# Kernel optimization log

Measured on AMD Instinct MI355X. Metric: run time of the kernel, lower is better.

Reference implementation:

```python
import jax, jax.numpy as jnp
import numpy as np

B = 1024       # batch of triples
E = 50000      # num_entities
R = 500        # num_relations
D = 512        # dimension
P = 16         # parts
C = 8          # num_cores
ALPHA = 2.0    # -> q = alpha/2 = 1.0
Q = ALPHA / 2.0
DP = D // P    # 32


def setup_inputs() -> dict:
    key = jax.random.key(0)
    ks = jax.random.split(key, 10)
    xav_e = (2.0 / (E + D)) ** 0.5
    xav_r = (2.0 / (R + D)) ** 0.5
    return {
        "heads": jax.random.randint(ks[0], (B,), 0, E),
        "relations": jax.random.randint(ks[1], (B,), 0, R),
        "tails": jax.random.randint(ks[2], (B,), 0, E),
        "entity_w": jax.random.normal(ks[3], (E, D), dtype=jnp.float32) * xav_e,
        "relation_w": jax.random.normal(ks[4], (R, D), dtype=jnp.float32) * xav_r,
        "W_cores": jax.random.uniform(ks[5], (C, P, P, P), dtype=jnp.float32,
                                      minval=-0.01, maxval=0.01),
        "attn_w1": jax.random.normal(ks[6], (2 * D, D), dtype=jnp.float32) * (1.0 / (2 * D)) ** 0.5,
        "attn_b1": jnp.zeros((D,), dtype=jnp.float32),
        "attn_w2": jax.random.normal(ks[7], (D, C), dtype=jnp.float32) * (1.0 / D) ** 0.5,
        "attn_b2": jnp.zeros((C,), dtype=jnp.float32),
    }


def _pq_norm(x):
    # ((|x|^p).sum(2) ** q).sum(1), p=2
    return ((x * x).sum(2) ** Q).sum(1)


def _geometric_consistency(W_cores):
    # center of mass of |W| along each axis, per core; vectorized over cores
    coords = jnp.arange(P, dtype=jnp.float32)
    Wa = jnp.abs(W_cores)                      # [C,P,P,P]
    tot = Wa.sum(axis=(1, 2, 3))               # [C]
    cx = (Wa * coords[None, :, None, None]).sum(axis=(1, 2, 3)) / tot
    cy = (Wa * coords[None, None, :, None]).sum(axis=(1, 2, 3)) / tot
    cz = (Wa * coords[None, None, None, :]).sum(axis=(1, 2, 3)) / tot
    centers = jnp.stack([cx, cy, cz], axis=1)  # [C,3]
    d2 = ((centers[:, None, :] - centers[None, :, :]) ** 2).sum(-1)
    dist = jnp.sqrt(d2)
    masked = dist + jnp.eye(C, dtype=dist.dtype) * 1e6
    min_d = masked.min(axis=1)
    return -jnp.mean(jnp.log(min_d + 1e-6))


def reference(heads, relations, tails, entity_w, relation_w, W_cores,
              attn_w1, attn_b1, attn_w2, attn_b2):
    h = entity_w[heads]          # [B,D]
    r = relation_w[relations]    # [B,D]
    t = entity_w[tails]          # [B,D]

    hr = jnp.concatenate([h, r], axis=1)                       # [B,2D]
    hid = jax.nn.relu(hr @ attn_w1 + attn_b1)                  # [B,D]
    attn = jax.nn.softmax(hid @ attn_w2 + attn_b2, axis=1)     # [B,C]

    h3 = h.reshape(-1, DP, P)
    r3 = r.reshape(-1, DP, P)
    t3 = t.reshape(-1, DP, P)

    h_norm = _pq_norm(h3)
    r_norm = _pq_norm(r3)
    t_norm = _pq_norm(t3)

    # attention-weighted effective core per triple (sum over cores is linear,
    # so folding attn into W before the contraction is exactly the same math)
    Weff = jnp.einsum('bc,cpqs->bpqs', attn, W_cores)          # [B,P,P,P]

    # x1[b,i,s] = sum_{p,q} h[b,i,p] r[b,i,q] W[b,p,q,s]
    x1 = jnp.einsum('bip,biq,bpqs->bis', h3, r3, Weff)
    # x2[b,i,p] = sum_{q,s} r[b,i,q] t[b,i,s] W[b,p,q,s]
    x2 = jnp.einsum('biq,bis,bpqs->bip', r3, t3, Weff)
    # x3[b,i,q] = sum_{p,s} h[b,i,p] t[b,i,s] W[b,p,q,s]
    x3 = jnp.einsum('bip,bis,bpqs->biq', h3, t3, Weff)

    whr_norm = _pq_norm(x1)
    wrt_norm = _pq_norm(x2)
    wth_norm = _pq_norm(x3)

    scores = x1.reshape(-1, D) @ entity_w.T                    # [B,E]

    factor1 = jnp.mean(h_norm) + jnp.mean(r_norm) + jnp.mean(t_norm)
    factor2 = jnp.mean(whr_norm) + jnp.mean(wrt_norm) + jnp.mean(wth_norm)
    factor3 = _geometric_consistency(W_cores)
    return (scores, factor1, factor2, factor3, attn)
```

## Files before the change

kernel.cpp:

```cpp
#include <hip/hip_runtime.h>
#include <cstdint>
#include <cstddef>

#define NB 1024
#define NE 50000
#define NE_PAD 50048
#define DCOL 512
#define ATTN_C 8

static const size_t SCORES_OFF = (size_t)NB * NE;
static const size_t F1_OFF = SCORES_OFF + 0;
static const size_t F2_OFF = SCORES_OFF + 1;
static const size_t F3_OFF = SCORES_OFF + 2;
static const size_t ATTN_OFF = SCORES_OFF + 3;

typedef float f32x4 __attribute__((ext_vector_type(4)));
typedef short s16x8 __attribute__((ext_vector_type(8)));

__device__ __forceinline__ unsigned short f2bf(float f) {
  union { float f; uint32_t u; } x; x.f = f;
  uint32_t u = x.u;
  uint32_t r = (u + 0x7fffu + ((u >> 16) & 1u)) >> 16;
  return (unsigned short)r;
}

__device__ __forceinline__ void gload16(const void* g, void* l) {
  __builtin_amdgcn_global_load_lds(
      (const __attribute__((address_space(1))) uint32_t*)g,
      (__attribute__((address_space(3))) uint32_t*)l, 16, 0, 0);
}

template <int N>
__device__ __forceinline__ void waitcnt_vm() {
  static_assert(N == 0 || N == 4 || N == 8, "literal dispatch");
  if constexpr (N == 0) asm volatile("s_waitcnt vmcnt(0)" ::: "memory");
  else if constexpr (N == 4) asm volatile("s_waitcnt vmcnt(4)" ::: "memory");
  else if constexpr (N == 8) asm volatile("s_waitcnt vmcnt(8)" ::: "memory");
}

__global__ __launch_bounds__(256)
void prep(const int* __restrict__ heads, const int* __restrict__ rels,
          const int* __restrict__ tails, const float* __restrict__ ew,
          const float* __restrict__ rw, const float* __restrict__ w1,
          unsigned short* __restrict__ hrb, unsigned short* __restrict__ w1t,
          unsigned short* __restrict__ ewb, float* __restrict__ n1) {
  int tid = threadIdx.x;
  if (blockIdx.x < NB) {
    int b = blockIdx.x;
    const float* h = ew + (size_t)heads[b] * DCOL;
    const float* r = rw + (size_t)rels[b] * DCOL;
    const float* t = ew + (size_t)tails[b] * DCOL;
    float acc = 0.f;
    #pragma unroll
    for (int it = 0; it < 2; ++it) {
      int d = it * 256 + tid;
      float hv = h[d], rv = r[d], tv = t[d];
      hrb[(size_t)b * 1024 + d] = f2bf(hv);
      hrb[(size_t)b * 1024 + DCOL + d] = f2bf(rv);
      acc += hv * hv + rv * rv + tv * tv;
    }
    __shared__ float red[256];
    red[tid] = acc; __syncthreads();
    for (int s = 128; s > 0; s >>= 1) {
      if (tid < s) red[tid] += red[tid + s];
      __syncthreads();
    }
    if (tid == 0) n1[b] = red[0];
  } else if (blockIdx.x < NB + 512) {
    int tb = blockIdx.x - NB;
    int nb = (tb & 15) * 32, kb = (tb >> 4) * 32;
    __shared__ float tile[32][33];
    int tx = tid & 31, ty = tid >> 5;
    #pragma unroll
    for (int rr = 0; rr < 32; rr += 8)
      tile[ty + rr][tx] = w1[(size_t)(kb + ty + rr) * 512 + nb + tx];
    __syncthreads();
    #pragma unroll
    for (int rr = 0; rr < 32; rr += 8)
      w1t[(size_t)(nb + ty + rr) * 1024 + kb + tx] = f2bf(tile[tx][ty + rr]);
  } else {
    const int n4valid = NE * DCOL / 4;
    const int n4tot = NE_PAD * DCOL / 4;
    int i = (blockIdx.x - NB - 512) * 256 + tid;
    const int stride = 2048 * 256;
    for (; i < n4tot; i += stride) {
      float x = 0.f, y = 0.f, z = 0.f, w = 0.f;
      if (i < n4valid) {
        float4 v = ((const float4*)ew)[i];
        x = v.x; y = v.y; z = v.z; w = v.w;
      }
      union { unsigned short u[4]; uint2 v2; } o;
      o.u[0] = f2bf(x); o.u[1] = f2bf(y); o.u[2] = f2bf(z); o.u[3] = f2bf(w);
      ((uint2*)ewb)[i] = o.v2;
    }
  }
}

template <int EPI, int WM, int WN, int FRm, int FRn, int SWZ, int MT>
__global__ __launch_bounds__(WM * WN * 64, WM * WN == 8 ? 4 : 2)
void gemm_nt(const unsigned short* __restrict__ A,
             const unsigned short* __restrict__ B,
             float* __restrict__ C, const float* __restrict__ bias,
             int K, int Nc, int NT) {
  constexpr int NW = WM * WN;
  constexpr int BM = WM * 16 * FRm;
  constexpr int BN = WN * 16 * FRn;
  constexpr int TILE_A = BM * 128;
  constexpr int TILE_B = BN * 128;
  constexpr int BUFSZ = TILE_A + TILE_B;
  constexpr int CPW_A = (BM / 8) / NW;
  constexpr int CPW_B = (BN / 8) / NW;
  constexpr int SOPS = CPW_A + CPW_B;
  static_assert((BM / 8) % NW == 0 && (BN / 8) % NW == 0, "chunk split");
  __shared__ __align__(16) uint8_t smem[2 * BUFSZ];
  const int tid = threadIdx.x;
  const int lane = tid & 63;
  const int wv = tid >> 6;
  const int wm = wv / WN, wn = wv % WN;

  int m_t, n_t;
  if (SWZ) {
    int xcd = blockIdx.x & 7;
    int l = blockIdx.x >> 3;
    int w = xcd * ((MT * NT) >> 3) + l;
    n_t = w / MT; m_t = w % MT;
  } else {
    m_t = blockIdx.x % MT; n_t = blockIdx.x / MT;
  }
  const int m0 = m_t * BM;
  const int n0 = n_t * BN;
  const int rbytes = K * 2;

  f32x4 acc[FRm][FRn];
  #pragma unroll
  for (int i = 0; i < FRm; ++i)
    #pragma unroll
    for (int j = 0; j < FRn; ++j) acc[i][j] = (f32x4){0.f, 0.f, 0.f, 0.f};

  const int srow = lane >> 3;
  const int scol = lane & 7;
  const int nkt = K >> 6;

  auto stage = [&](int kt, int buf) {
    #pragma unroll
    for (int j = 0; j < CPW_A; ++j) {
      const int chunk = wv * CPW_A + j;
      const int r = chunk * 8 + srow;
      const int c = scol ^ (r & 7);
      gload16((const uint8_t*)A + (size_t)(m0 + r) * rbytes + kt * 128 + c * 16,
              &smem[buf * BUFSZ + chunk * 1024]);
    }
    #pragma unroll
    for (int j = 0; j < CPW_B; ++j) {
      const int chunk = wv * CPW_B + j;
      const int r = chunk * 8 + srow;
      const int c = scol ^ (r & 7);
      gload16((const uint8_t*)B + (size_t)(n0 + r) * rbytes + kt * 128 + c * 16,
              &smem[buf * BUFSZ + TILE_A + chunk * 1024]);
    }
  };
  auto compute = [&](int buf) {
    const uint8_t* sa = &smem[buf * BUFSZ];
    const uint8_t* sb = sa + TILE_A;
    #pragma unroll
    for (int kk = 0; kk < 2; ++kk) {
      s16x8 af[FRm], bfv[FRn];
      #pragma unroll
      for (int f = 0; f < FRm; ++f) {
        const int ra = (wm * FRm + f) * 16 + (lane & 15);
        const int ca = (kk * 4 + (lane >> 4)) ^ (ra & 7);
        af[f] = *(const s16x8*)&sa[ra * 128 + ca * 16];
      }
      #pragma unroll
      for (int f = 0; f < FRn; ++f) {
        const int rb = (wn * FRn + f) * 16 + (lane & 15);
        const int cb = (kk * 4 + (lane >> 4)) ^ (rb & 7);
        bfv[f] = *(const s16x8*)&sb[rb * 128 + cb * 16];
      }
      #pragma unroll
      for (int fm = 0; fm < FRm; ++fm)
        #pragma unroll
        for (int fn = 0; fn < FRn; ++fn)
          acc[fm][fn] = __builtin_amdgcn_mfma_f32_16x16x32_bf16(
              af[fm], bfv[fn], acc[fm][fn], 0, 0, 0);
    }
  };

  stage(0, 0);
  stage(1, 1);
  for (int kt = 0; kt < nkt - 1; ++kt) {
    const int cur = kt & 1;
    waitcnt_vm<SOPS>();
    __builtin_amdgcn_sched_barrier(0);
    __builtin_amdgcn_s_barrier();
    __builtin_amdgcn_sched_barrier(0);
    compute(cur);
    __builtin_amdgcn_sched_barrier(0);
    __builtin_amdgcn_s_barrier();
    __builtin_amdgcn_sched_barrier(0);
    if (kt + 2 < nkt) stage(kt + 2, cur);
  }
  waitcnt_vm<0>();
  __builtin_amdgcn_sched_barrier(0);
  __builtin_amdgcn_s_barrier();
  __builtin_amdgcn_sched_barrier(0);
  compute((nkt - 1) & 1);

  const int rl = lane >> 4, cl = lane & 15;
  #pragma unroll
  for (int fm = 0; fm < FRm; ++fm)
    #pragma unroll
    for (int fn = 0; fn < FRn; ++fn)
      #pragma unroll
      for (int j = 0; j < 4; ++j) {
        int gm = m0 + (wm * FRm + fm) * 16 + rl * 4 + j;
        int gn = n0 + (wn * FRn + fn) * 16 + cl;
        if (gn < Nc) {
          float v = acc[fm][fn][j];
          if (EPI) v = fmaxf(v + bias[gn], 0.f);
          C[(size_t)gm * Nc + gn] = v;
        }
      }
}

__global__ __launch_bounds__(256, 2)
void triple_core(const int* __restrict__ heads, const int* __restrict__ rels,
                 const int* __restrict__ tails, const float* __restrict__ ew,
                 const float* __restrict__ rw, const float* __restrict__ wc,
                 const float* __restrict__ hid, const float* __restrict__ w2,
                 const float* __restrict__ b2, float* __restrict__ attn_out,
                 unsigned short* __restrict__ x1b, float* __restrict__ n2) {
  __shared__ float hs[512], rs[512], ts[512];
  __shared__ __align__(16) float W123[4096][4];
  __shared__ float att[8];
  __shared__ float wred[4][8];
  __shared__ float red[256];
  int b = blockIdx.x, tid = threadIdx.x;
  int lane = tid & 63, wid = tid >> 6;
  const float* hp_ = ew + (size_t)heads[b] * DCOL;
  const float* rp_ = rw + (size_t)rels[b] * DCOL;
  const float* tp_ = ew + (size_t)tails[b] * DCOL;
  float la[8] = {0, 0, 0, 0, 0, 0, 0, 0};
  #pragma unroll
  for (int it = 0; it < 2; ++it) {
    int d = it * 256 + tid;
    hs[d] = hp_[d]; rs[d] = rp_[d]; ts[d] = tp_[d];
    float hv = hid[(size_t)b * DCOL + d];
    #pragma unroll
    for (int c = 0; c < 8; ++c) la[c] = fmaf(hv, w2[d * 8 + c], la[c]);
  }
  #pragma unroll
  for (int off = 32; off > 0; off >>= 1)
    #pragma unroll
    for (int c = 0; c < 8; ++c) la[c] += __shfl_down(la[c], off);
  if (lane == 0)
    #pragma unroll
    for (int c = 0; c < 8; ++c) wred[wid][c] = la[c];
  __syncthreads();
  if (tid == 0) {
    float lg[8];
    #pragma unroll
    for (int c = 0; c < 8; ++c)
      lg[c] = wred[0][c] + wred[1][c] + wred[2][c] + wred[3][c] + b2[c];
    float mx = lg[0];
    #pragma unroll
    for (int c = 1; c < 8; ++c) mx = fmaxf(mx, lg[c]);
    float e[8], s = 0.f;
    #pragma unroll
    for (int c = 0; c < 8; ++c) { e[c] = expf(lg[c] - mx); s += e[c]; }
    #pragma unroll
    for (int c = 0; c < 8; ++c) {
      float a = e[c] / s;
      att[c] = a;
      attn_out[(size_t)b * 8 + c] = a;
    }
  }
  __syncthreads();
  #pragma unroll
  for (int it = 0; it < 16; ++it) {
    int idx = it * 256 + tid;
    float w = 0.f;
    #pragma unroll
    for (int c = 0; c < 8; ++c) w = fmaf(att[c], wc[c * 4096 + idx], w);
    int s = idx & 15, q = (idx >> 4) & 15, p = idx >> 8;
    W123[idx][0] = w;
    W123[(q * 16 + s) * 16 + p][1] = w;
    W123[(p * 16 + s) * 16 + q][2] = w;
  }
  __syncthreads();

  const int so = tid & 15;
  const int i0 = tid >> 4, i1 = i0 + 16;
  float h0[16], r0[16], t0[16], h1[16], r1[16], t1[16];
  #pragma unroll
  for (int k = 0; k < 16; ++k) {
    h0[k] = hs[i0 * 16 + k]; r0[k] = rs[i0 * 16 + k]; t0[k] = ts[i0 * 16 + k];
    h1[k] = hs[i1 * 16 + k]; r1[k] = rs[i1 * 16 + k]; t1[k] = ts[i1 * 16 + k];
  }
  float a10 = 0.f, a20 = 0.f, a30 = 0.f, a11 = 0.f, a21 = 0.f, a31 = 0.f;
  const float4* wp = (const float4*)&W123[so][0];
  #pragma unroll
  for (int u = 0; u < 16; ++u) {
    #pragma unroll
    for (int v = 0; v < 16; ++v) {
      float4 w = wp[u * 256 + v * 16];
      a10 = fmaf(h0[u] * r0[v], w.x, a10);
      a20 = fmaf(r0[u] * t0[v], w.y, a20);
      a30 = fmaf(h0[u] * t0[v], w.z, a30);
      a11 = fmaf(h1[u] * r1[v], w.x, a11);
      a21 = fmaf(r1[u] * t1[v], w.y, a21);
      a31 = fmaf(h1[u] * t1[v], w.z, a31);
    }
  }
  x1b[(size_t)b * 512 + i0 * 16 + so] = f2bf(a10);
  x1b[(size_t)b * 512 + i1 * 16 + so] = f2bf(a11);
  red[tid] = a10 * a10 + a20 * a20 + a30 * a30
           + a11 * a11 + a21 * a21 + a31 * a31;
  __syncthreads();
  for (int s = 128; s > 0; s >>= 1) {
    if (tid < s) red[tid] += red[tid + s];
    __syncthreads();
  }
  if (tid == 0) n2[b] = red[0];
}

__global__ __launch_bounds__(256)
void finalize(const float* __restrict__ n1, const float* __restrict__ n2,
              const float* __restrict__ wc, float* __restrict__ out) {
  int tid = threadIdx.x;
  __shared__ float red[256];
  float a = 0.f;
  for (int i = tid; i < NB; i += 256) a += n1[i];
  red[tid] = a; __syncthreads();
  for (int s = 128; s > 0; s >>= 1) { if (tid < s) red[tid] += red[tid + s]; __syncthreads(); }
  if (tid == 0) out[F1_OFF] = red[0] / (float)NB;
  __syncthreads();
  a = 0.f;
  for (int i = tid; i < NB; i += 256) a += n2[i];
  red[tid] = a; __syncthreads();
  for (int s = 128; s > 0; s >>= 1) { if (tid < s) red[tid] += red[tid + s]; __syncthreads(); }
  if (tid == 0) out[F2_OFF] = red[0] / (float)NB;
  __syncthreads();

  int c = tid >> 5, l = tid & 31;
  float tot = 0.f, cx = 0.f, cy = 0.f, cz = 0.f;
  for (int e = l; e < 4096; e += 32) {
    float w = fabsf(wc[c * 4096 + e]);
    int z = e & 15, y = (e >> 4) & 15, x = e >> 8;
    tot += w; cx += w * x; cy += w * y; cz += w * z;
  }
  #pragma unroll
  for (int off = 16; off > 0; off >>= 1) {
    tot += __shfl_down(tot, off);
    cx += __shfl_down(cx, off);
    cy += __shfl_down(cy, off);
    cz += __shfl_down(cz, off);
  }
  __shared__ float cent[8][3];
  if (l == 0) { cent[c][0] = cx / tot; cent[c][1] = cy / tot; cent[c][2] = cz / tot; }
  __syncthreads();
  if (tid == 0) {
    float f3 = 0.f;
    for (int i = 0; i < 8; ++i) {
      float mn = 1e30f;
      for (int j = 0; j < 8; ++j) {
        if (j == i) continue;
        float dx = cent[i][0] - cent[j][0];
        float dy = cent[i][1] - cent[j][1];
        float dz = cent[i][2] - cent[j][2];
        float d = sqrtf(dx * dx + dy * dy + dz * dz);
        mn = fminf(mn, d);
      }
      f3 += logf(mn + 1e-6f);
    }
    out[F3_OFF] = -f3 / 8.f;
  }
}

extern "C" void kernel_launch(void* const* d_in, const int* in_sizes, int n_in,
                              void* d_out, int out_size, void* d_ws, size_t ws_size,
                              hipStream_t stream) {
  const int* heads = (const int*)d_in[0];
  const int* rels = (const int*)d_in[1];
  const int* tails = (const int*)d_in[2];
  const float* ew = (const float*)d_in[3];
  const float* rw = (const float*)d_in[4];
  const float* wc = (const float*)d_in[5];
  const float* w1 = (const float*)d_in[6];
  const float* b1 = (const float*)d_in[7];
  const float* w2 = (const float*)d_in[8];
  const float* b2 = (const float*)d_in[9];
  float* out = (float*)d_out;

  uint8_t* ws = (uint8_t*)d_ws;
  const size_t EWB_SZ = (size_t)NE_PAD * DCOL * 2;
  unsigned short* ewb = (unsigned short*)ws;
  unsigned short* hrb = (unsigned short*)(ws + EWB_SZ);
  unsigned short* w1t = (unsigned short*)(ws + EWB_SZ + 2097152);
  float* hid = (float*)(ws + EWB_SZ + 2097152 + 1048576);
  unsigned short* x1b = (unsigned short*)(ws + EWB_SZ + 2097152 + 1048576 + 2097152);
  float* n1 = (float*)(ws + EWB_SZ + 2097152 + 1048576 + 2097152 + 1048576);
  float* n2 = n1 + NB;

  prep<<<NB + 512 + 2048, 256, 0, stream>>>(heads, rels, tails, ew, rw, w1,
                                            hrb, w1t, ewb, n1);
  gemm_nt<1, 2, 2, 2, 2, 0, 16><<<128, 256, 0, stream>>>(
      hrb, w1t, hid, b1, 1024, 512, 8);
  triple_core<<<NB, 256, 0, stream>>>(heads, rels, tails, ew, rw, wc,
                                      hid, w2, b2, out + ATTN_OFF, x1b, n2);
  gemm_nt<0, 2, 4, 4, 2, 1, 8><<<3128, 512, 0, stream>>>(
      x1b, ewb, out, nullptr, 512, NE, 391);
  finalize<<<1, 256, 0, stream>>>(n1, n2, wc, out);
}
```

Before: 215.2 us.

## Overlap entity bf16 conversion with attention GEMM and reshape scores GEMM warps

The fp32-to-bf16 conversion of the entity table moves out of the prep kernel and into extra blocks of the attention hidden-layer GEMM launch. Those blocks run alongside the small 128-block GEMM, so the bandwidth-bound conversion overlaps with compute that barely fills the device. The scores GEMM also changes from 8 warps with 4x2 fragments to 4 warps with 4x4 fragments, keeping a 128x128 tile. Launch bounds drop to a fixed minimum of 2 blocks. The extra conversion blocks add a branch to the GEMM kernel and may compete with it for memory bandwidth.

```diff
diff --git a/kernel.cpp b/kernel.cpp
--- a/kernel.cpp
+++ b/kernel.cpp
@@ -43,7 +43,7 @@
           const int* __restrict__ tails, const float* __restrict__ ew,
           const float* __restrict__ rw, const float* __restrict__ w1,
           unsigned short* __restrict__ hrb, unsigned short* __restrict__ w1t,
-          unsigned short* __restrict__ ewb, float* __restrict__ n1) {
+          float* __restrict__ n1) {
   int tid = threadIdx.x;
   if (blockIdx.x < NB) {
     int b = blockIdx.x;
@@ -66,7 +66,7 @@
       __syncthreads();
     }
     if (tid == 0) n1[b] = red[0];
-  } else if (blockIdx.x < NB + 512) {
+  } else {
     int tb = blockIdx.x - NB;
     int nb = (tb & 15) * 32, kb = (tb >> 4) * 32;
     __shared__ float tile[32][33];
@@ -78,30 +78,17 @@
     #pragma unroll
     for (int rr = 0; rr < 32; rr += 8)
       w1t[(size_t)(nb + ty + rr) * 1024 + kb + tx] = f2bf(tile[tx][ty + rr]);
-  } else {
-    const int n4valid = NE * DCOL / 4;
-    const int n4tot = NE_PAD * DCOL / 4;
-    int i = (blockIdx.x - NB - 512) * 256 + tid;
-    const int stride = 2048 * 256;
-    for (; i < n4tot; i += stride) {
-      float x = 0.f, y = 0.f, z = 0.f, w = 0.f;
-      if (i < n4valid) {
-        float4 v = ((const float4*)ew)[i];
-        x = v.x; y = v.y; z = v.z; w = v.w;
-      }
-      union { unsigned short u[4]; uint2 v2; } o;
-      o.u[0] = f2bf(x); o.u[1] = f2bf(y); o.u[2] = f2bf(z); o.u[3] = f2bf(w);
-      ((uint2*)ewb)[i] = o.v2;
-    }
-  }
-}
-
-template <int EPI, int WM, int WN, int FRm, int FRn, int SWZ, int MT>
-__global__ __launch_bounds__(WM * WN * 64, WM * WN == 8 ? 4 : 2)
+  }
+}
+
+template <int EPI, int WM, int WN, int FRm, int FRn, int SWZ, int MT, int CVT>
+__global__ __launch_bounds__(WM * WN * 64, 2)
 void gemm_nt(const unsigned short* __restrict__ A,
              const unsigned short* __restrict__ B,
              float* __restrict__ C, const float* __restrict__ bias,
-             int K, int Nc, int NT) {
+             int K, int Nc, int NT,
+             const float* __restrict__ cvt_src,
+             unsigned short* __restrict__ cvt_dst, int ngemm) {
   constexpr int NW = WM * WN;
   constexpr int BM = WM * 16 * FRm;
   constexpr int BN = WN * 16 * FRn;
@@ -114,6 +101,25 @@
   static_assert((BM / 8) % NW == 0 && (BN / 8) % NW == 0, "chunk split");
   __shared__ __align__(16) uint8_t smem[2 * BUFSZ];
   const int tid = threadIdx.x;
+
+  if (CVT && (int)blockIdx.x >= ngemm) {
+    const int n4valid = NE * DCOL / 4;
+    const int n4tot = NE_PAD * DCOL / 4;
+    int i = ((int)blockIdx.x - ngemm) * (NW * 64) + tid;
+    const int stride = ((int)gridDim.x - ngemm) * (NW * 64);
+    for (; i < n4tot; i += stride) {
+      float x = 0.f, y = 0.f, z = 0.f, w = 0.f;
+      if (i < n4valid) {
+        float4 v = ((const float4*)cvt_src)[i];
+        x = v.x; y = v.y; z = v.z; w = v.w;
+      }
+      union { unsigned short u[4]; uint2 v2; } o;
+      o.u[0] = f2bf(x); o.u[1] = f2bf(y); o.u[2] = f2bf(z); o.u[3] = f2bf(w);
+      ((uint2*)cvt_dst)[i] = o.v2;
+    }
+    return;
+  }
+
   const int lane = tid & 63;
   const int wv = tid >> 6;
   const int wm = wv / WN, wn = wv % WN;
@@ -402,13 +408,13 @@
   float* n1 = (float*)(ws + EWB_SZ + 2097152 + 1048576 + 2097152 + 1048576);
   float* n2 = n1 + NB;
 
-  prep<<<NB + 512 + 2048, 256, 0, stream>>>(heads, rels, tails, ew, rw, w1,
-                                            hrb, w1t, ewb, n1);
-  gemm_nt<1, 2, 2, 2, 2, 0, 16><<<128, 256, 0, stream>>>(
-      hrb, w1t, hid, b1, 1024, 512, 8);
+  prep<<<NB + 512, 256, 0, stream>>>(heads, rels, tails, ew, rw, w1,
+                                     hrb, w1t, n1);
+  gemm_nt<1, 2, 2, 2, 2, 0, 16, 1><<<128 + 2048, 256, 0, stream>>>(
+      hrb, w1t, hid, b1, 1024, 512, 8, ew, ewb, 128);
   triple_core<<<NB, 256, 0, stream>>>(heads, rels, tails, ew, rw, wc,
                                       hid, w2, b2, out + ATTN_OFF, x1b, n2);
-  gemm_nt<0, 2, 4, 4, 2, 1, 8><<<3128, 512, 0, stream>>>(
-      x1b, ewb, out, nullptr, 512, NE, 391);
+  gemm_nt<0, 2, 2, 4, 4, 1, 8, 0><<<3128, 256, 0, stream>>>(
+      x1b, ewb, out, nullptr, 512, NE, 391, nullptr, nullptr, 0);
   finalize<<<1, 256, 0, stream>>>(n1, n2, wc, out);
 }
```

Measured after the change: 214.8 us. Within noise of the previous version (-0.2%).
